# Kernel optimization log

Hardware: AMD Instinct MI355X
Metric: run time of the kernel (lower is better)

The kernel has to match this reference:

```python
import jax, jax.numpy as jnp
import numpy as np

M = 12          # persons per frame
K = 2           # partition channels from conv1da (1024 = 2*512)
D = 512         # GCN channel dim / LSTM hidden
C_IN = 4096     # backbone feature dim
NUM_CLASSES = 8


def setup_inputs() -> dict:
    key = jax.random.key(0)
    ks = jax.random.split(key, 8)
    N, T = 16, 32
    NT = N * T
    base_out = jax.random.normal(ks[0], (NT, M, C_IN), dtype=jnp.float32)
    dist = jax.random.uniform(ks[1], (N, T, 3, K, M, M), dtype=jnp.float32)
    # conv1da: Conv1d(4096 -> 1024, k=1, bias=False) == matmul with [1024, 4096]
    w_a = jax.random.normal(ks[2], (K * D, C_IN), dtype=jnp.float32) * 0.02
    # LSTM(512, 512, 1): torch gate order i, f, g, o
    s = 1.0 / np.sqrt(D)
    w_ih = jax.random.uniform(ks[3], (4 * D, D), minval=-s, maxval=s, dtype=jnp.float32)
    w_hh = jax.random.uniform(ks[4], (4 * D, D), minval=-s, maxval=s, dtype=jnp.float32)
    b_ih = jax.random.uniform(ks[5], (4 * D,), minval=-s, maxval=s, dtype=jnp.float32)
    b_hh = jax.random.uniform(ks[6], (4 * D,), minval=-s, maxval=s, dtype=jnp.float32)
    # gclassifier: Linear(512 -> num_classes)
    w_cls = jax.random.normal(ks[7], (NUM_CLASSES, D), dtype=jnp.float32) * 0.01
    b_cls = jnp.zeros((NUM_CLASSES,), dtype=jnp.float32)
    return {"base_out": base_out, "dist": dist, "w_a": w_a,
            "w_ih": w_ih, "w_hh": w_hh, "b_ih": b_ih, "b_hh": b_hh,
            "w_cls": w_cls, "b_cls": b_cls, "n_videos": N}


def reference(base_out, dist, w_a, w_ih, w_hh, b_ih, b_hh, w_cls, b_cls, n_videos):
    NT = base_out.shape[0]
    N = n_videos
    T = NT // N
    # conv1da (1x1 conv, no bias): [NT, M, 4096] -> [NT, K*D, M] -> [NT, K, D, M]
    node1 = jnp.einsum('nmc,oc->nom', base_out, w_a).reshape(NT, K, D, M)
    # fused three-way adjacency aggregation: node1a + node1b + node1c
    A = (dist[:, :, 2] + dist[:, :, 1] + dist[:, :, 0]).reshape(NT, K, M, M)
    node = jnp.einsum('nkcv,nkvw->ncw', node1, A)  # [NT, D, M]
    node = jax.nn.relu(node)
    # AdaptiveAvgPool1d(1) over the M persons
    pooled = node.mean(axis=2)                      # [NT, D]
    seq = pooled.reshape(N, T, D)
    # torch nn.LSTM default batch_first=False: iterates over axis 0 (N), batch=T
    def step(carry, x_t):
        h, c = carry
        g = x_t @ w_ih.T + b_ih + h @ w_hh.T + b_hh  # [T, 4D]
        i, f, gg, o = jnp.split(g, 4, axis=-1)
        c = jax.nn.sigmoid(f) * c + jax.nn.sigmoid(i) * jnp.tanh(gg)
        h = jax.nn.sigmoid(o) * jnp.tanh(c)
        return (h, c), h
    h0 = jnp.zeros((T, D), dtype=seq.dtype)
    c0 = jnp.zeros((T, D), dtype=seq.dtype)
    _, hs = jax.lax.scan(step, (h0, c0), seq)       # [N, T, D]
    last = hs[:, -1, :]                              # video_feat[:, -1, :]
    return last @ w_cls.T + b_cls                    # [N, num_classes]
```

## Files before the change

kernel.cpp:

```cpp
#include <hip/hip_runtime.h>
#include <math.h>

#define MM 12
#define KK 2
#define DD 512
#define CIN 4096
#define NCLS 8
#define NV 16
#define TT 32

typedef unsigned long long u64;
typedef __attribute__((ext_vector_type(8))) __bf16 bf16x8;
typedef __attribute__((ext_vector_type(4))) float f32x4;

#define PART_F   0
#define POOLED_F 786432
#define TAGGX_F  794752
#define HGLOB_F  796800
#define GX_F     813184
#define PART_KS_STRIDE (192 * 1024)

#define MFMA_BF16(A, B, C) __builtin_amdgcn_mfma_f32_16x16x32_bf16((A), (B), (C), 0, 0, 0)
#define LOADR(p)      __hip_atomic_load((p), __ATOMIC_RELAXED, __HIP_MEMORY_SCOPE_AGENT)
#define LOADACQ(p)    __hip_atomic_load((p), __ATOMIC_ACQUIRE, __HIP_MEMORY_SCOPE_AGENT)
#define STOREREL(p, v) __hip_atomic_store((p), (v), __ATOMIC_RELEASE, __HIP_MEMORY_SCOPE_AGENT)
#define LOADS(p)      __hip_atomic_load((p), __ATOMIC_RELAXED, __HIP_MEMORY_SCOPE_SYSTEM)
#define EXCHS(p, v)   (void)__hip_atomic_exchange((p), (v), __ATOMIC_RELAXED, __HIP_MEMORY_SCOPE_SYSTEM)

static __device__ __forceinline__ u64 ld_sc0(const u64* p) {
  u64 v;
  asm volatile("global_load_dwordx2 %0, %1, off sc0\n\ts_waitcnt vmcnt(0)"
               : "=v"(v) : "v"(p) : "memory");
  return v;
}
static __device__ __forceinline__ void st_sc0(u64* p, u64 v) {
  asm volatile("global_store_dwordx2 %0, %1, off sc0" :: "v"(p), "v"(v) : "memory");
}

static __device__ __forceinline__ void cvt_store(
    unsigned short* __restrict__ hb, unsigned short* __restrict__ lb,
    int idx, float4 v) {
  unsigned ux = __float_as_uint(v.x), uy = __float_as_uint(v.y);
  unsigned uz = __float_as_uint(v.z), uw = __float_as_uint(v.w);
  *(uint2*)&hb[idx] = make_uint2((ux >> 16) | (uy & 0xFFFF0000u),
                                 (uz >> 16) | (uw & 0xFFFF0000u));
  unsigned lx = __float_as_uint(v.x - __uint_as_float(ux & 0xFFFF0000u));
  unsigned ly = __float_as_uint(v.y - __uint_as_float(uy & 0xFFFF0000u));
  unsigned lz = __float_as_uint(v.z - __uint_as_float(uz & 0xFFFF0000u));
  unsigned lw = __float_as_uint(v.w - __uint_as_float(uw & 0xFFFF0000u));
  *(uint2*)&lb[idx] = make_uint2((lx >> 16) | (ly & 0xFFFF0000u),
                                 (lz >> 16) | (lw & 0xFFFF0000u));
}

__global__ __launch_bounds__(64, 1) void k_gemm(
    const float* __restrict__ base_out, const float* __restrict__ w_a,
    float* __restrict__ part)
{
  const int wg = blockIdx.x;
  const int ks = wg & 3;
  const int ot = (wg >> 2) & 63;
  const int jq = wg >> 8;
  const int cc0 = ks * 1024;
  const int lane = threadIdx.x;

  __shared__ __align__(16) unsigned short Ah0[16 * 40], Al0[16 * 40];
  __shared__ __align__(16) unsigned short Bh0[16 * 40], Bl0[16 * 40];
  __shared__ __align__(16) unsigned short Ah1[16 * 40], Al1[16 * 40];
  __shared__ __align__(16) unsigned short Bh1[16 * 40], Bl1[16 * 40];

  const int sq = lane & 7;
  const int sr = lane >> 3;

  unsigned boffA[2], boffB[2], aoffA[2], aoffB[2];
#pragma unroll
  for (int rep = 0; rep < 2; ++rep) {
    const int j = jq * 16 + sr + 8 * rep;
    const int n = j / 12, m = j - n * 12;
    boffA[rep] = (unsigned)(((n * TT + 31) * MM + m) * CIN + cc0 + sq * 4);
    boffB[rep] = boffA[rep] + 32;
    aoffA[rep] = (unsigned)((ot * 16 + sr + 8 * rep) * CIN + cc0 + sq * 4);
    aoffB[rep] = aoffA[rep] + 32;
  }

  f32x4 acc0 = {0.f, 0.f, 0.f, 0.f};

  float4 paA[2], pbA[2], paB[2], pbB[2];
#pragma unroll
  for (int r2 = 0; r2 < 2; ++r2) {
    paA[r2] = *(const float4*)&w_a[aoffA[r2]];
    pbA[r2] = *(const float4*)&base_out[boffA[r2]];
    paB[r2] = *(const float4*)&w_a[aoffB[r2]];
    pbB[r2] = *(const float4*)&base_out[boffB[r2]];
  }

#define STAGE_TO(AH, AL, BH, BL, PA, PB)                                    \
  {                                                                         \
    _Pragma("unroll")                                                       \
    for (int r2 = 0; r2 < 2; ++r2)                                          \
      cvt_store(AH, AL, (sr + 8 * r2) * 40 + sq * 4, PA[r2]);               \
    _Pragma("unroll")                                                       \
    for (int r2 = 0; r2 < 2; ++r2)                                          \
      cvt_store(BH, BL, (sr + 8 * r2) * 40 + sq * 4, PB[r2]);               \
  }
#define LOAD_SET(PA, PB, AOFF, BOFF)                                        \
  {                                                                         \
    _Pragma("unroll")                                                       \
    for (int r2 = 0; r2 < 2; ++r2) {                                        \
      AOFF[r2] += 64; PA[r2] = *(const float4*)&w_a[AOFF[r2]];              \
      BOFF[r2] += 64; PB[r2] = *(const float4*)&base_out[BOFF[r2]];         \
    }                                                                       \
  }
#define CONSUME(AH, AL, BH, BL)                                             \
  {                                                                         \
    const int koff = (lane >> 4) * 8;                                       \
    const int fra = (lane & 15) * 40 + koff;                                \
    bf16x8 oh = *(const bf16x8*)&AH[fra];                                   \
    bf16x8 ol = *(const bf16x8*)&AL[fra];                                   \
    bf16x8 jh = *(const bf16x8*)&BH[fra];                                   \
    bf16x8 jl = *(const bf16x8*)&BL[fra];                                   \
    acc0 = MFMA_BF16(jh, oh, acc0);                                         \
    acc0 = MFMA_BF16(jh, ol, acc0);                                         \
    acc0 = MFMA_BF16(jl, oh, acc0);                                         \
  }

  STAGE_TO(Ah0, Al0, Bh0, Bl0, paA, pbA);
  LOAD_SET(paA, pbA, aoffA, boffA);

  for (int st = 0; st < 32; st += 2) {
    STAGE_TO(Ah1, Al1, Bh1, Bl1, paB, pbB);
    if (st + 3 < 32) LOAD_SET(paB, pbB, aoffB, boffB);
    CONSUME(Ah0, Al0, Bh0, Bl0);
    if (st + 2 < 32) STAGE_TO(Ah0, Al0, Bh0, Bl0, paA, pbA);
    if (st + 4 < 32) LOAD_SET(paA, pbA, aoffA, boffA);
    CONSUME(Ah1, Al1, Bh1, Bl1);
  }
#undef STAGE_TO
#undef LOAD_SET
#undef CONSUME

  const int o = ot * 16 + (lane & 15);
  const int jr = (lane >> 4) * 4;
#pragma unroll
  for (int r = 0; r < 4; ++r)
    part[((size_t)ks * 192 + jq * 16 + jr + r) * 1024 + o] = acc0[r];
}

__global__ __launch_bounds__(256, 1) void k_pool(
    const float* __restrict__ dist, const float* __restrict__ part,
    float* __restrict__ pooled)
{
  const int wg = blockIdx.x;
  const int tid = threadIdx.x;

  __shared__ float Asum_s[KK * MM * MM];

  const int n = wg >> 4, cb = (wg & 15) * 32;
  const unsigned dbase = (unsigned)((n * TT + 31) * (3 * KK * MM * MM));
  for (int f = tid; f < KK * MM * MM; f += 256)
    Asum_s[f] = dist[dbase + f] + dist[dbase + KK * MM * MM + f]
              + dist[dbase + 2 * KK * MM * MM + f];
  __syncthreads();
  if (tid < 32) {
    const int c = cb + tid;
    float nd[KK][MM];
#pragma unroll
    for (int k = 0; k < KK; ++k)
#pragma unroll
      for (int v = 0; v < MM; ++v) {
        const size_t off = (size_t)(n * MM + v) * 1024 + k * DD + c;
        nd[k][v] = part[off] + part[off + PART_KS_STRIDE]
                 + part[off + 2 * PART_KS_STRIDE] + part[off + 3 * PART_KS_STRIDE];
      }
    float accm = 0.f;
#pragma unroll
    for (int w = 0; w < MM; ++w) {
      float sw = 0.f;
#pragma unroll
      for (int k = 0; k < KK; ++k)
#pragma unroll
        for (int v = 0; v < MM; ++v) sw += nd[k][v] * Asum_s[(k * MM + v) * MM + w];
      accm += fmaxf(sw, 0.f);
    }
    pooled[n * DD + c] = accm * (1.f / 12.f);
  }
}

__global__ __launch_bounds__(1024, 1) void k_rest(
    const float* __restrict__ pooled,
    const float* __restrict__ w_ih, const float* __restrict__ w_hh,
    const float* __restrict__ b_ih, const float* __restrict__ b_hh,
    const float* __restrict__ w_cls, const float* __restrict__ b_cls,
    unsigned* __restrict__ tagGX, float* __restrict__ gxg,
    u64* __restrict__ hg64, float* __restrict__ out)
{
  const int wg = blockIdx.x;
  const int tid = threadIdx.x;

  __shared__ __align__(16) float whh_s[64][516];
  __shared__ float gx_s[16][64];
  __shared__ __align__(16) float h_s[DD];
  __shared__ float dot_s[64];
  __shared__ float gxp_s[1024];

  if ((wg & 7) != 0) {
    const int k = wg & 7;
    if (k > 4) return;
    const int m = wg >> 3;
    const int dd = m + 32 * (k - 1);
    {
      const int q4 = tid >> 8;
      const int r = tid & 255;
      const int n = r & 15, j = r >> 4;
      const int gr = dd * 16 + j;
      const float4* wr = (const float4*)&w_ih[(size_t)gr * DD];
      const float4* pv = (const float4*)&pooled[(size_t)n * DD];
      float a = 0.f;
#pragma unroll 8
      for (int q = q4 * 32; q < q4 * 32 + 32; ++q) {
        float4 x = wr[q], y = pv[q];
        a += x.x * y.x + x.y * y.y + x.z * y.z + x.w * y.w;
      }
      gxp_s[tid] = a;
    }
    __syncthreads();
    if (tid < 256) {
      const int n = tid & 15, j = tid >> 4;
      const int gr = dd * 16 + j;
      const float a = ((gxp_s[tid] + gxp_s[tid + 256]) + gxp_s[tid + 512])
                    + gxp_s[tid + 768] + b_ih[gr] + b_hh[gr];
      gxg[m * 1024 + n * 64 + (k - 1) * 16 + j] = a;
    }
    __syncthreads();
    if (tid == 0) STOREREL(&tagGX[dd * 16], 1u);
    return;
  }

  const int w = wg >> 3;
  float c_reg = 0.f;

  for (int f = tid; f < 64 * 128; f += 1024) {
    const int rr = f >> 7, c4 = (f & 127) * 4;
    const int grow = (rr >> 4) * DD + w * 16 + (rr & 15);
    *(float4*)&whh_s[rr][c4] = *(const float4*)&w_hh[(size_t)grow * DD + c4];
  }
  if (tid < 64) {
    bool done;
    do {
      int t0 = (int)LOADR(&tagGX[(w + 32 * (tid & 3)) * 16]);
      done = __all(t0 == 1);
    } while (!done);
  }
  __syncthreads();
  gx_s[tid >> 6][tid & 63] =
      __uint_as_float(LOADS((const unsigned*)&gxg[w * 1024 + tid]));
  __syncthreads();

  if (tid < 16) {
    const float pi = gx_s[0][tid]      + 0.0f;
    const float pf = gx_s[0][16 + tid] + 0.0f;
    const float pg = gx_s[0][32 + tid] + 0.0f;
    const float po = gx_s[0][48 + tid] + 0.0f;
    const float si = 1.f / (1.f + expf(-pi));
    const float sf = 1.f / (1.f + expf(-pf));
    const float so = 1.f / (1.f + expf(-po));
    c_reg = sf * c_reg + si * tanhf(pg);
    const float hn = so * tanhf(c_reg);
    const u64 pk = ((u64)__float_as_uint(hn) << 32) | (u64)1u;
    u64* pp = &hg64[w * 16 + tid];
    st_sc0(pp, pk);
    EXCHS(pp, pk);
  }
  __syncthreads();

  {
    const int r = tid >> 4;
    const int lj = tid & 15;

    for (int s = 1; s < NV; ++s) {
      if (tid < DD) {
        const u64* p = &hg64[(size_t)(s - 1) * DD + tid];
        u64 v = ld_sc0(p);
        while ((unsigned)v != (unsigned)s) {
          v = LOADS(p);
          if ((unsigned)v == (unsigned)s) break;
          v = ld_sc0(p);
        }
        h_s[tid] = __uint_as_float((unsigned)(v >> 32));
      }
      __syncthreads();

      float p = 0.f;
      const float4* wrow = (const float4*)&whh_s[r][0];
      const float4* hv4 = (const float4*)h_s;
#pragma unroll
      for (int q = 0; q < 8; ++q) {
        float4 wv = wrow[lj + 16 * q];
        float4 hv = hv4[lj + 16 * q];
        p += wv.x * hv.x + wv.y * hv.y + wv.z * hv.z + wv.w * hv.w;
      }
#pragma unroll
      for (int off = 8; off; off >>= 1) p += __shfl_down(p, off, 16);
      if (lj == 0) dot_s[r] = p;
      __syncthreads();

      if (tid < 16) {
        const float pi = gx_s[s][tid]      + dot_s[tid];
        const float pf = gx_s[s][16 + tid] + dot_s[16 + tid];
        const float pg = gx_s[s][32 + tid] + dot_s[32 + tid];
        const float po = gx_s[s][48 + tid] + dot_s[48 + tid];
        const float si = 1.f / (1.f + expf(-pi));
        const float sf = 1.f / (1.f + expf(-pf));
        const float so = 1.f / (1.f + expf(-po));
        c_reg = sf * c_reg + si * tanhf(pg);
        const float hn = so * tanhf(c_reg);
        const u64 pk = ((u64)__float_as_uint(hn) << 32) | (u64)(unsigned)(s + 1);
        u64* pp = &hg64[(size_t)s * DD + w * 16 + tid];
        st_sc0(pp, pk);
        EXCHS(pp, pk);
      }
    }
  }

  if (wg == 0) {
    float* scratch = &whh_s[0][0];
    if (tid < DD) {
      u64 vv[NV];
#pragma unroll
      for (int n = 0; n < NV; ++n) vv[n] = LOADS(&hg64[(size_t)n * DD + tid]);
#pragma unroll
      for (int n = 0; n < NV; ++n) {
        u64 v = vv[n];
        while ((unsigned)v != (unsigned)(n + 1))
          v = LOADS(&hg64[(size_t)n * DD + tid]);
        scratch[n * 516 + tid] = __uint_as_float((unsigned)(v >> 32));
      }
    }
    __syncthreads();
    if (tid < NV * NCLS) {
      const int n = tid >> 3, cl = tid & 7;
      const float4* hv = (const float4*)&scratch[n * 516];
      const float4* wv = (const float4*)(w_cls + (size_t)cl * DD);
      float a = b_cls[cl];
#pragma unroll 8
      for (int q = 0; q < DD / 4; ++q) {
        float4 x = hv[q], y = wv[q];
        a += x.x * y.x + x.y * y.y + x.z * y.z + x.w * y.w;
      }
      out[tid] = a;
    }
  }
}

extern "C" void kernel_launch(void* const* d_in, const int* in_sizes, int n_in,
                              void* d_out, int out_size, void* d_ws, size_t ws_size,
                              hipStream_t stream) {
  const float* base_out = (const float*)d_in[0];
  const float* dist     = (const float*)d_in[1];
  const float* w_a      = (const float*)d_in[2];
  const float* w_ih     = (const float*)d_in[3];
  const float* w_hh     = (const float*)d_in[4];
  const float* b_ih     = (const float*)d_in[5];
  const float* b_hh     = (const float*)d_in[6];
  const float* w_cls    = (const float*)d_in[7];
  const float* b_cls    = (const float*)d_in[8];
  float* out = (float*)d_out;

  float* ws = (float*)d_ws;
  float* part   = ws + PART_F;
  float* pooled = ws + POOLED_F;
  unsigned* tagGX = (unsigned*)(ws + TAGGX_F);
  u64* hg64 = (u64*)(ws + HGLOB_F);
  float* gxg = ws + GX_F;

  k_gemm<<<dim3(3072), 64, 0, stream>>>(base_out, w_a, part);
  k_pool<<<dim3(256), 256, 0, stream>>>(dist, part, pooled);
  k_rest<<<dim3(256), 1024, 0, stream>>>(pooled, w_ih, w_hh, b_ih, b_hh,
                                         w_cls, b_cls, tagGX, gxg, hg64, out);
}
```

Measured before the change: 251.2 us.

## Replace per-step block barriers in LSTM recurrence with tagged LDS flag handoff

The LSTM recurrence loop now passes h and the partial dot products through double-buffered shared-memory slots, each tagged with its step number. Waves spin on those tags instead of using __syncthreads, so the two block-wide barriers per timestep are gone. Dedicated waves (tid>=512) fetch remote h values from global memory, and the local workgroup's own h is written straight to LDS. This removes barrier latency from the serial critical path, at the cost of spin-polling LDS and relying on workgroup-scope atomic ordering being correct.

```diff
diff --git a/kernel.cpp b/kernel.cpp
--- a/kernel.cpp
+++ b/kernel.cpp
@@ -26,6 +26,8 @@
 #define STOREREL(p, v) __hip_atomic_store((p), (v), __ATOMIC_RELEASE, __HIP_MEMORY_SCOPE_AGENT)
 #define LOADS(p)      __hip_atomic_load((p), __ATOMIC_RELAXED, __HIP_MEMORY_SCOPE_SYSTEM)
 #define EXCHS(p, v)   (void)__hip_atomic_exchange((p), (v), __ATOMIC_RELAXED, __HIP_MEMORY_SCOPE_SYSTEM)
+#define ALD(p)        __hip_atomic_load((p), __ATOMIC_RELAXED, __HIP_MEMORY_SCOPE_WORKGROUP)
+#define AST(p, v)     __hip_atomic_store((p), (v), __ATOMIC_RELAXED, __HIP_MEMORY_SCOPE_WORKGROUP)
 
 static __device__ __forceinline__ u64 ld_sc0(const u64* p) {
   u64 v;
@@ -35,6 +37,12 @@
 }
 static __device__ __forceinline__ void st_sc0(u64* p, u64 v) {
   asm volatile("global_store_dwordx2 %0, %1, off sc0" :: "v"(p), "v"(v) : "memory");
+}
+static __device__ __forceinline__ float hval(u64 v) {
+  return __uint_as_float((unsigned)(v >> 32));
+}
+static __device__ __forceinline__ u64 packf(float x, int tag) {
+  return ((u64)__float_as_uint(x) << 32) | (u64)(unsigned)tag;
 }
 
 static __device__ __forceinline__ void cvt_store(
@@ -198,9 +206,9 @@
 
   __shared__ __align__(16) float whh_s[64][516];
   __shared__ float gx_s[16][64];
-  __shared__ __align__(16) float h_s[DD];
-  __shared__ float dot_s[64];
   __shared__ float gxp_s[1024];
+  __shared__ __align__(8) u64 hl[2][DD];
+  __shared__ __align__(8) u64 dl[2][64];
 
   if ((wg & 7) != 0) {
     const int k = wg & 7;
@@ -255,6 +263,10 @@
       __uint_as_float(LOADS((const unsigned*)&gxg[w * 1024 + tid]));
   __syncthreads();
 
+  for (int f = tid; f < 2 * DD; f += 1024) ((u64*)hl)[f] = 0;
+  if (tid < 128) ((u64*)dl)[tid] = 0;
+  __syncthreads();
+
   if (tid < 16) {
     const float pi = gx_s[0][tid]      + 0.0f;
     const float pf = gx_s[0][16 + tid] + 0.0f;
@@ -265,55 +277,68 @@
     const float so = 1.f / (1.f + expf(-po));
     c_reg = sf * c_reg + si * tanhf(pg);
     const float hn = so * tanhf(c_reg);
-    const u64 pk = ((u64)__float_as_uint(hn) << 32) | (u64)1u;
+    const u64 pk = packf(hn, 1);
+    AST(&hl[1][w * 16 + tid], pk);
     u64* pp = &hg64[w * 16 + tid];
     st_sc0(pp, pk);
     EXCHS(pp, pk);
   }
-  __syncthreads();
 
   {
     const int r = tid >> 4;
     const int lj = tid & 15;
+    const int gd = tid - 512;
+    const bool gact = (tid >= 512) && ((gd >> 4) != w);
 
     for (int s = 1; s < NV; ++s) {
-      if (tid < DD) {
-        const u64* p = &hg64[(size_t)(s - 1) * DD + tid];
-        u64 v = ld_sc0(p);
+      const int par = s & 1;
+      if (gact) {
+        const u64* gp = &hg64[(size_t)(s - 1) * DD + gd];
+        u64 v = ld_sc0(gp);
         while ((unsigned)v != (unsigned)s) {
-          v = LOADS(p);
+          v = LOADS(gp);
           if ((unsigned)v == (unsigned)s) break;
-          v = ld_sc0(p);
+          v = ld_sc0(gp);
         }
-        h_s[tid] = __uint_as_float((unsigned)(v >> 32));
-      }
-      __syncthreads();
-
-      float p = 0.f;
+        AST(&hl[par][gd], v);
+      }
+      float acc = 0.f;
       const float4* wrow = (const float4*)&whh_s[r][0];
-      const float4* hv4 = (const float4*)h_s;
 #pragma unroll
       for (int q = 0; q < 8; ++q) {
-        float4 wv = wrow[lj + 16 * q];
-        float4 hv = hv4[lj + 16 * q];
-        p += wv.x * hv.x + wv.y * hv.y + wv.z * hv.z + wv.w * hv.w;
-      }
-#pragma unroll
-      for (int off = 8; off; off >>= 1) p += __shfl_down(p, off, 16);
-      if (lj == 0) dot_s[r] = p;
-      __syncthreads();
+        const int a = lj + 16 * q;
+        const u64* hp = &hl[par][4 * a];
+        u64 v0, v1, v2, v3;
+        do {
+          v0 = ALD(&hp[0]); v1 = ALD(&hp[1]);
+          v2 = ALD(&hp[2]); v3 = ALD(&hp[3]);
+        } while (((unsigned)v0 != (unsigned)s) | ((unsigned)v1 != (unsigned)s) |
+                 ((unsigned)v2 != (unsigned)s) | ((unsigned)v3 != (unsigned)s));
+        const float4 wv = wrow[a];
+        acc += wv.x * hval(v0) + wv.y * hval(v1) + wv.z * hval(v2) + wv.w * hval(v3);
+      }
+#pragma unroll
+      for (int off = 8; off; off >>= 1) acc += __shfl_down(acc, off, 16);
+      if (lj == 0) AST(&dl[par][r], packf(acc, s));
 
       if (tid < 16) {
-        const float pi = gx_s[s][tid]      + dot_s[tid];
-        const float pf = gx_s[s][16 + tid] + dot_s[16 + tid];
-        const float pg = gx_s[s][32 + tid] + dot_s[32 + tid];
-        const float po = gx_s[s][48 + tid] + dot_s[48 + tid];
+        u64 d0, d1, d2, d3;
+        do {
+          d0 = ALD(&dl[par][tid]);      d1 = ALD(&dl[par][16 + tid]);
+          d2 = ALD(&dl[par][32 + tid]); d3 = ALD(&dl[par][48 + tid]);
+        } while (((unsigned)d0 != (unsigned)s) | ((unsigned)d1 != (unsigned)s) |
+                 ((unsigned)d2 != (unsigned)s) | ((unsigned)d3 != (unsigned)s));
+        const float pi = gx_s[s][tid]      + hval(d0);
+        const float pf = gx_s[s][16 + tid] + hval(d1);
+        const float pg = gx_s[s][32 + tid] + hval(d2);
+        const float po = gx_s[s][48 + tid] + hval(d3);
         const float si = 1.f / (1.f + expf(-pi));
         const float sf = 1.f / (1.f + expf(-pf));
         const float so = 1.f / (1.f + expf(-po));
         c_reg = sf * c_reg + si * tanhf(pg);
         const float hn = so * tanhf(c_reg);
-        const u64 pk = ((u64)__float_as_uint(hn) << 32) | (u64)(unsigned)(s + 1);
+        const u64 pk = packf(hn, s + 1);
+        AST(&hl[(s + 1) & 1][w * 16 + tid], pk);
         u64* pp = &hg64[(size_t)s * DD + w * 16 + tid];
         st_sc0(pp, pk);
         EXCHS(pp, pk);
@@ -322,6 +347,7 @@
   }
 
   if (wg == 0) {
+    __syncthreads();
     float* scratch = &whh_s[0][0];
     if (tid < DD) {
       u64 vv[NV];
```

Measured after the change: 264.8 us. +5.4%, slower.
